# Performance work log

Hardware: AMD Instinct MI355X
Metric: run time of the kernel (lower is better)

## Reference

```python
import jax, jax.numpy as jnp
import numpy as np

# ---- static config (matches init_kwargs: nlevs=[2,3,4], Pyr_mode=1, dfilt='pkva') ----
NLEVS = (2, 3, 4)
L = 3
# symmetric length-12 ladder (lifting) filter in the spirit of the 'pkva' ladder filter
_PKVA_HALF = np.array([0.6300, -0.1930, 0.0972, -0.0526, 0.0272, -0.0144])
PKVA = np.concatenate([_PKVA_HALF[::-1], _PKVA_HALF])


def _lp_hp_masks(H, W):
    """Meyer-style smooth lowpass/highpass frequency masks (rcos smooth_func)."""
    def phi(n):
        w = np.abs(2.0 * np.pi * np.fft.fftfreq(n))
        s = np.clip((w - np.pi / 3.0) / (np.pi / 3.0), 0.0, 1.0)
        beta = s ** 4 * (35.0 - 84.0 * s + 70.0 * s ** 2 - 20.0 * s ** 3)
        return np.cos(0.5 * np.pi * beta)
    Lm = phi(H)[:, None] * phi(W)[None, :]
    Hm = np.sqrt(np.clip(1.0 - Lm ** 2, 0.0, None))
    return jnp.asarray(Lm, jnp.float32), jnp.asarray(Hm, jnp.float32)


def _pyr_dec(x, nlev):
    """PyrNDDEC_mm, Pyr_mode=1: FFT-domain smooth LP/HP split, dyadic decimation of LP."""
    bands = []
    for _ in range(nlev):
        H, W = x.shape[-2], x.shape[-1]
        Lm, Hm = _lp_hp_masks(H, W)
        Xf = jnp.fft.fft2(x)
        bands.append(jnp.fft.ifft2(Xf * Hm).real.astype(x.dtype))
        x = jnp.fft.ifft2(Xf * Lm).real.astype(x.dtype)[..., ::2, ::2]
    return [x] + bands[::-1]  # y[0]=coarsest lowpass, y[1..L]=bandpass coarse->fine


def _conv1d_wrap(x, f, axis):
    """1D circular ('wrap') convolution along `axis`."""
    K = f.shape[0]
    x = jnp.moveaxis(x, axis, -1)
    pad = [(0, 0)] * (x.ndim - 1) + [(K // 2, K - 1 - K // 2)]
    xp = jnp.pad(x, pad, mode='wrap')
    shp = xp.shape
    y = jax.lax.conv_general_dilated(xp.reshape(-1, 1, shp[-1]),
                                     f.reshape(1, 1, K).astype(x.dtype), (1,), 'VALID')
    y = y.reshape(shp[:-1] + (shp[-1] - K + 1,))
    return jnp.moveaxis(y, -1, axis)


def _fan_split(x, axis, f):
    """One ladder-structured fan filter-bank stage with quincunx coset split."""
    other = -2 if axis == -1 else -1
    n_other = x.shape[other]
    shape = [1] * x.ndim
    shape[other] = n_other
    idx = jnp.arange(n_other)
    # fan <-> diamond modulation along the other axis
    sign = (1 - 2 * (idx % 2)).astype(x.dtype).reshape(shape)
    xm = x * sign
    # quincunx cosets: shift odd lines by 1 along split axis, then deinterleave
    parity = ((idx % 2) == 1).reshape(shape)
    xs = jnp.where(parity, jnp.roll(xm, -1, axis=axis), xm)
    if axis == -1:
        p0, p1 = xs[..., 0::2], xs[..., 1::2]
    else:
        p0, p1 = xs[..., 0::2, :], xs[..., 1::2, :]
    # ladder (lifting) predict/update with 1D filter f
    d = p1 - _conv1d_wrap(p0, f, axis)
    s = p0 + 0.5 * _conv1d_wrap(d, f, axis)
    return s, d


def _dfbdec(x, f, n):
    """n-level directional filter bank (ladder structure). Returns (2^n, ...) stack."""
    subs = x[None]  # (M, B, 1, H, W), all subbands same shape per level -> vectorized
    axis = -1
    for _ in range(n):
        s, d = _fan_split(subs, axis, f)
        subs = jnp.concatenate([s, d], axis=0)
        axis = -2 if axis == -1 else -1
    return subs


def setup_inputs() -> dict:
    key = jax.random.key(0)
    x = jax.random.normal(key, (16, 1, 1024, 1024), dtype=jnp.float32)
    return {"x": x}


def reference(x):
    f = jnp.asarray(PKVA, x.dtype)
    y = _pyr_dec(x, L)
    outs = [y[0]]  # coarsest lowpass (B,1,128,128)
    for k in range(1, L + 1):
        outs.append(_dfbdec(y[k], f, NLEVS[k - 1]))
    # (lowpass, 4 dirs @128x128, 8 dirs @(256,128), 16 dirs @(256,256))
    return tuple(outs)
```

## Files before the change

kernel.cpp:

```cpp
#include <hip/hip_runtime.h>
#include <math.h>

#define PI_F 3.14159265358979323846f

__constant__ float c_pkva[12] = {
  -0.0144f, 0.0272f, -0.0526f, 0.0972f, -0.193f, 0.63f,
   0.63f, -0.193f, 0.0972f, -0.0526f, 0.0272f, -0.0144f
};

constexpr int ilog2c(int n) { int l = 0; while (n > 1) { n >>= 1; ++l; } return l; }

__device__ float g_phi[1920];
__device__ float2 g_tw[512];
constexpr int phi_off(int N) {
  return (N == 1024) ? 0 : (N == 512) ? 1024 : (N == 256) ? 1536 : 1792;
}

__device__ __forceinline__ float phi_dev(int k, int n) {
  int kk = (k < n - k) ? k : (n - k);
  float w = 2.0f * PI_F * (float)kk / (float)n;
  float s = (w - PI_F / 3.0f) * (3.0f / PI_F);
  s = fminf(fmaxf(s, 0.0f), 1.0f);
  float s2 = s * s;
  float beta = s2 * s2 * (35.0f - 84.0f * s + 70.0f * s2 - 20.0f * s2 * s);
  return __cosf(0.5f * PI_F * beta);
}

__global__ void phi_init_k() {
  int i = blockIdx.x * 256 + threadIdx.x;
  if (i < 1024)      g_phi[i] = phi_dev(i, 1024);
  else if (i < 1536) g_phi[i] = phi_dev(i - 1024, 512);
  else if (i < 1792) g_phi[i] = phi_dev(i - 1536, 256);
  else if (i < 1920) g_phi[i] = phi_dev(i - 1792, 128);
  else {
    int idx = i - 1920;
    if (idx >= 1 && idx < 512) {
      int l = 31 - __clz(idx);
      int Ns = 1 << l;
      float th = 2.0f * PI_F * (float)(idx - Ns) / (float)(4 * Ns);
      g_tw[idx] = make_float2(cosf(th), sinf(th));
    }
  }
}

__device__ __forceinline__ float2 cmul(float2 a, float2 b) {
  return make_float2(a.x * b.x - a.y * b.y, a.x * b.y + a.y * b.x);
}
__device__ __forceinline__ float2 cadd(float2 a, float2 b) { return make_float2(a.x + b.x, a.y + b.y); }
__device__ __forceinline__ float2 csub(float2 a, float2 b) { return make_float2(a.x - b.x, a.y - b.y); }

template <int N>
__device__ __forceinline__ int fft_core4(float2 (*sbuf)[N], float dirsign, int tid, int cur) {
  constexpr int LOG2 = ilog2c(N);
  constexpr int NT = N / 4;
  constexpr bool LEAD2 = (LOG2 & 1);
  if constexpr (LEAD2) {
#pragma unroll
    for (int j = tid; j < N / 2; j += NT) {
      float2 v0 = sbuf[cur][j], v1 = sbuf[cur][j + N / 2];
      float2 e = cadd(v0, v1), o = csub(v0, v1);
      *(float4*)&sbuf[cur ^ 1][2 * j] = make_float4(e.x, e.y, o.x, o.y);
    }
    cur ^= 1;
    __syncthreads();
  }
#pragma unroll
  for (int Ns = LEAD2 ? 2 : 1; Ns < N; Ns <<= 2) {
    int j = tid;
    int base = j & (Ns - 1);
    float2 t = g_tw[Ns + base];
    float2 w1 = make_float2(t.x, dirsign * t.y);
    float2 w2 = cmul(w1, w1);
    float2 w3 = cmul(w2, w1);
    float2 v0 = sbuf[cur][j];
    float2 v1 = cmul(sbuf[cur][j + N / 4], w1);
    float2 v2 = cmul(sbuf[cur][j + N / 2], w2);
    float2 v3 = cmul(sbuf[cur][j + 3 * (N / 4)], w3);
    float2 a0 = cadd(v0, v2), a1 = csub(v0, v2);
    float2 a2 = cadd(v1, v3), a3 = csub(v1, v3);
    float2 r1 = make_float2(-dirsign * a3.y, dirsign * a3.x);
    int idxD = ((j - base) << 2) + base;
    cur ^= 1;
    sbuf[cur][idxD]          = cadd(a0, a2);
    sbuf[cur][idxD + Ns]     = cadd(a1, r1);
    sbuf[cur][idxD + 2 * Ns] = csub(a0, a2);
    sbuf[cur][idxD + 3 * Ns] = csub(a1, r1);
    __syncthreads();
  }
  return cur;
}

template <int N, int LMODE, int SMODE>
__global__ void __launch_bounds__(N / 4)
fft_rows_k(const void* __restrict__ vin, void* __restrict__ vout,
           float dirsign, float scale) {
  constexpr int NT = N / 4;
  __shared__ __align__(16) float2 sbuf[2][N];
  const int tid = threadIdx.x;
  const int row = blockIdx.x;
  const int r = row & (N - 1);

  if (LMODE == 1) {
    const float2* in = (const float2*)vin;
#pragma unroll
    for (int i = tid; i < N; i += NT) {
      float2 v = in[(size_t)row * N + i];
      sbuf[0][i] = make_float2(v.x * scale, v.y * scale);
    }
  } else {
    const float2* in = (const float2*)vin;
    float pr = g_phi[phi_off(N) + r];
#pragma unroll
    for (int i = tid; i < N; i += NT) {
      float lm = pr * g_phi[phi_off(N) + i];
      float m = sqrtf(fmaxf(1.0f - lm * lm, 0.0f)) * scale;
      float2 v = in[(size_t)row * N + i];
      sbuf[0][i] = make_float2(v.x * m, v.y * m);
    }
  }
  __syncthreads();

  int cur = fft_core4<N>(sbuf, dirsign, tid, 0);

  if (SMODE == 0) {
    float2* outp = (float2*)vout;
#pragma unroll
    for (int i = tid; i < N; i += NT)
      outp[(size_t)row * N + i] = sbuf[cur][i];
  } else {
    float* outp = (float*)vout;
#pragma unroll
    for (int i = tid; i < N; i += NT)
      outp[(size_t)row * N + i] = sbuf[cur][i].x;
  }
}

template <int N, int LMODE>
__global__ void __launch_bounds__(N / 4)
fft_rows_cm_k(const float2* __restrict__ in, float2* __restrict__ outcm,
              float scale) {
  constexpr int NT = N / 4;
  __shared__ __align__(16) float2 sbuf[2][N];
  const int tid = threadIdx.x;
  const int img = blockIdx.y;
  const int b = blockIdx.x;
  const int q = ((b & 7) << (ilog2c(N) - 4)) + (b >> 3);
  float2 r0v[4], r1v[4];

#pragma unroll
  for (int half = 0; half < 2; ++half) {
    const int r = 2 * q + half;
    if constexpr (LMODE == 1) {
      const float2* rp = in + ((size_t)img * N + r) * N;
#pragma unroll
      for (int i = tid; i < N; i += NT) {
        float2 v = rp[i];
        sbuf[0][i] = make_float2(v.x * scale, v.y * scale);
      }
    } else if constexpr (LMODE == 2) {
      const float2* rp = in + ((size_t)img * N + r) * N;
      float pr = g_phi[phi_off(N) + r];
#pragma unroll
      for (int i = tid; i < N; i += NT) {
        float lm = pr * g_phi[phi_off(N) + i];
        float m = sqrtf(fmaxf(1.0f - lm * lm, 0.0f)) * scale;
        float2 v = rp[i];
        sbuf[0][i] = make_float2(v.x * m, v.y * m);
      }
    } else {
      const float2* fb = in + (size_t)img * (513 * 512);
      const float2* fr0 = fb + (size_t)r * 512;
      const float2* fr1 = fb + (size_t)(512 - r) * 512;
      float pr = g_phi[phi_off(512) + r];
#pragma unroll
      for (int i = tid; i < N; i += NT) {
        float2 a = fr0[i], bb = fr1[(512 - i) & 511];
        float lm = pr * g_phi[phi_off(512) + i];
        float m = sqrtf(fmaxf(1.0f - lm * lm, 0.0f)) * scale;
        sbuf[0][i] = make_float2((a.x + bb.x) * m, (a.y - bb.y) * m);
      }
    }
    __syncthreads();

    int cur = fft_core4<N>(sbuf, 1.0f, tid, 0);

#pragma unroll
    for (int k = 0; k < 4; ++k) {
      int i = tid + k * NT;
      if (i < N) {
        float2 v = sbuf[cur][i];
        if (half == 0) r0v[k] = v; else r1v[k] = v;
      }
    }
    __syncthreads();
  }

  float2* ob = outcm + (size_t)img * N * N + 2 * q;
#pragma unroll
  for (int k = 0; k < 4; ++k) {
    int i = tid + k * NT;
    if (i < N)
      *(float4*)&ob[(size_t)i * N] = make_float4(r0v[k].x, r0v[k].y, r1v[k].x, r1v[k].y);
  }
}

template <int N, int PITCH>
__global__ void __launch_bounds__(N / 4)
rfft_pairs_cm_k(const float* __restrict__ in, float2* __restrict__ out) {
  constexpr int NT = N / 4;
  __shared__ __align__(16) float2 sbuf[2][N];
  const int tid = threadIdx.x;
  const int img = blockIdx.x >> (ilog2c(N) - 1);
  const int b = blockIdx.x & (N / 2 - 1);
  const int r = ((b & 7) << (ilog2c(N) - 4)) + (b >> 3);
  const float* p0 = in + ((size_t)img * N + 2 * r) * N;
  const float* p1 = p0 + N;

#pragma unroll
  for (int i = tid; i < N; i += NT)
    sbuf[0][i] = make_float2(p0[i], p1[i]);
  __syncthreads();

  int cur = fft_core4<N>(sbuf, -1.0f, tid, 0);

  float2* ob = out + (size_t)img * ((size_t)PITCH * N) + 2 * r;
#pragma unroll
  for (int i = tid; i <= N / 2; i += NT) {
    float2 Z = sbuf[cur][i];
    float2 Zr = sbuf[cur][(N - i) & (N - 1)];
    float2 Zc = make_float2(Zr.x, -Zr.y);
    float2 o0 = make_float2(0.5f * (Z.x + Zc.x), 0.5f * (Z.y + Zc.y));
    float2 dd = make_float2(Z.x - Zc.x, Z.y - Zc.y);
    float2 o1 = make_float2(0.5f * dd.y, -0.5f * dd.x);
    *(float4*)&ob[(size_t)i * N] = make_float4(o0.x, o0.y, o1.x, o1.y);
  }
}

template <int N, int PITCH>
__global__ void __launch_bounds__(N / 4)
fft_col_half_pair_k(const float2* __restrict__ in, float2* __restrict__ outT,
                    float2* __restrict__ foldb) {
  constexpr int NT = N / 4;
  constexpr int NH = N / 2;
  constexpr int NP = N / 4;
  __shared__ __align__(16) float2 sbuf[2][N];
  const int tid = threadIdx.x;
  const int img = blockIdx.y;
  const int b = blockIdx.x;
  const int t = (b < NP) ? (((b & 7) * (NP / 8)) + (b >> 3)) : NP;
  const float inv = 1.0f / (float)N;
  float2 k0[4], k1[4];

#pragma unroll 1
  for (int half = 0; half < 2; ++half) {
    const int kx = 2 * t + half;
    if (kx > NH) break;
    const float2* rowp = in + ((size_t)img * PITCH + kx) * N;
#pragma unroll
    for (int i = tid; i < N; i += NT)
      sbuf[0][i] = rowp[i];
    __syncthreads();

    int cur = fft_core4<N>(sbuf, -1.0f, tid, 0);

    const float pr = g_phi[phi_off(N) + kx];
    float2* fp = foldb + ((size_t)img * (NH + 1) + kx) * NH;
#pragma unroll
    for (int i = tid; i < NH; i += NT) {
      float2 vA = sbuf[cur][i];
      float2 vB = sbuf[cur][i + NH];
      float lmA = pr * g_phi[phi_off(N) + i];
      float lmB = pr * g_phi[phi_off(N) + i + NH];
      fp[i] = make_float2(0.25f * (vA.x * lmA + vB.x * lmB),
                          0.25f * (vA.y * lmA + vB.y * lmB));
      float hmA = sqrtf(fmaxf(1.0f - lmA * lmA, 0.0f)) * inv;
      float hmB = sqrtf(fmaxf(1.0f - lmB * lmB, 0.0f)) * inv;
      sbuf[cur][i]      = make_float2(vA.x * hmA, vA.y * hmA);
      sbuf[cur][i + NH] = make_float2(vB.x * hmB, vB.y * hmB);
    }
    __syncthreads();

    cur = fft_core4<N>(sbuf, 1.0f, tid, cur);

#pragma unroll
    for (int k = 0; k < 4; ++k) {
      int i = tid + k * NT;
      float2 v = sbuf[cur][i];
      if (half == 0) k0[k] = v; else k1[k] = v;
    }
    __syncthreads();
  }

  if (t < NP) {
#pragma unroll
    for (int k = 0; k < 4; ++k) {
      int i = tid + k * NT;
      *(float4*)&outT[((size_t)img * N + i) * PITCH + 2 * t] =
          make_float4(k0[k].x, k0[k].y, k1[k].x, k1[k].y);
    }
  } else {
#pragma unroll
    for (int k = 0; k < 4; ++k) {
      int i = tid + k * NT;
      outT[((size_t)img * N + i) * PITCH + NH] = k0[k];
    }
  }
}

__global__ void __launch_bounds__(256)
fold_spec3_k(const float2* __restrict__ fold, float2* __restrict__ spec3) {
  __shared__ float2 s2a[512], s2b[512];
  const int rp = blockIdx.x;
  const int img = blockIdx.y;
  const float2* fb = fold + (size_t)img * (513 * 512);
  const float2* fr0 = fb + (size_t)rp * 512;
  const float2* fr1 = fb + (size_t)(512 - rp) * 512;
  const float2* fr2 = fb + (size_t)(rp + 256) * 512;
  const float2* fr3 = fb + (size_t)(256 - rp) * 512;
  for (int c = threadIdx.x; c < 512; c += 256) {
    int mc = (512 - c) & 511;
    float2 a0 = fr0[c], b0 = fr1[mc];
    float2 a1 = fr2[c], b1 = fr3[mc];
    s2a[c] = make_float2(a0.x + b0.x, a0.y - b0.y);
    s2b[c] = make_float2(a1.x + b1.x, a1.y - b1.y);
  }
  __syncthreads();
  float pr0 = g_phi[phi_off(512) + rp], pr1 = g_phi[phi_off(512) + rp + 256];
  float2* sp3 = spec3 + ((size_t)img << 16) + ((size_t)rp << 8);
  {
    int c = threadIdx.x;
    float pc0 = g_phi[phi_off(512) + c], pc1 = g_phi[phi_off(512) + c + 256];
    float2 v00 = s2a[c], v01 = s2a[c + 256], v10 = s2b[c], v11 = s2b[c + 256];
    float m00 = pr0 * pc0, m01 = pr0 * pc1, m10 = pr1 * pc0, m11 = pr1 * pc1;
    sp3[c] = make_float2(
        0.25f * (v00.x * m00 + v01.x * m01 + v10.x * m10 + v11.x * m11),
        0.25f * (v00.y * m00 + v01.y * m01 + v10.y * m10 + v11.y * m11));
  }
}

template <int N, int PITCH>
__global__ void __launch_bounds__(N / 4)
ifft_fan_pair_k(const float2* __restrict__ in, float* __restrict__ outb,
                float scale, int halfT) {
  constexpr int NT = N / 4;
  constexpr int W2 = N / 2;
  __shared__ __align__(16) float2 sbuf[2][N];
  const int tid = threadIdx.x;
  const int img = blockIdx.x >> (ilog2c(N) - 1);
  const int q = blockIdx.x & (N / 2 - 1);
  const int y0 = 2 * q;
  const float2* inA = in + ((size_t)img * N + y0) * PITCH;
  const float2* inB = inA + PITCH;

#pragma unroll
  for (int i = tid; i <= W2; i += NT) {
    float2 a = inA[i], b = inB[i];
    sbuf[0][i] = make_float2((a.x - b.y) * scale, (a.y + b.x) * scale);
  }
#pragma unroll
  for (int i = tid; i < W2 - 1; i += NT) {
    int m = W2 - 1 - i;
    float2 a = inA[m], b = inB[m];
    sbuf[0][W2 + 1 + i] = make_float2((a.x + b.y) * scale, (b.x - a.y) * scale);
  }
  __syncthreads();

  int cur = fft_core4<N>(sbuf, 1.0f, tid, 0);

  float* scratch = (float*)sbuf[cur ^ 1];
  float* xe = scratch;
  float* xo = scratch + W2;
  float* db = scratch + 2 * W2;
  const size_t rbase = ((size_t)img * N + y0) * W2;

  for (int sub = 0; sub < 2; ++sub) {
    const int par = sub;
    const float sgn = par ? -1.0f : 1.0f;
#pragma unroll
    for (int i = tid; i < N; i += NT) {
      float v = par ? sbuf[cur][i].y : sbuf[cur][i].x;
      int ii = (i - par) & (N - 1);
      if (ii & 1) xo[ii >> 1] = v; else xe[ii >> 1] = v;
    }
    __syncthreads();

    float* outs = outb + rbase + (size_t)sub * W2;
    float* outd = outb + halfT + rbase + (size_t)sub * W2;
#pragma unroll 2
    for (int j = tid; j < W2; j += NT) {
      float acc = 0.0f;
#pragma unroll
      for (int k = 0; k < 12; k++)
        acc += c_pkva[k] * xe[(j - 6 + k + W2) & (W2 - 1)];
      float dv = sgn * (xo[j] - acc);
      db[j] = dv;
      outd[j] = dv;
    }
    __syncthreads();
#pragma unroll 2
    for (int j = tid; j < W2; j += NT) {
      float acc = 0.0f;
#pragma unroll
      for (int k = 0; k < 12; k++)
        acc += c_pkva[k] * db[(j - 6 + k + W2) & (W2 - 1)];
      outs[j] = sgn * xe[j] + 0.5f * acc;
    }
    __syncthreads();
  }
}

template <int N>
__global__ void __launch_bounds__(N / 4)
ifft_fan_k(const float2* __restrict__ in, float* __restrict__ outb,
           float scale, int halfT) {
  constexpr int NT = N / 4;
  constexpr int W2 = N / 2;
  __shared__ __align__(16) float2 sbuf[2][N];
  const int tid = threadIdx.x;
  const int nr = blockIdx.x;
  const int r = nr & (N - 1);
  const int par = r & 1;
  const float sgn = par ? -1.0f : 1.0f;

#pragma unroll
  for (int i = tid; i < N; i += NT) {
    float2 v = in[(size_t)nr * N + i];
    sbuf[0][i] = make_float2(v.x * scale, v.y * scale);
  }
  __syncthreads();

  int cur = fft_core4<N>(sbuf, 1.0f, tid, 0);

  float* scratch = (float*)sbuf[cur ^ 1];
  float* xe = scratch;
  float* xo = scratch + W2;
  float* db = scratch + 2 * W2;
#pragma unroll
  for (int i = tid; i < N; i += NT) {
    float v = sbuf[cur][i].x;
    int ii = (i - par) & (N - 1);
    if (ii & 1) xo[ii >> 1] = v; else xe[ii >> 1] = v;
  }
  __syncthreads();

  float* outs = outb + (size_t)nr * W2;
  float* outd = outb + halfT + (size_t)nr * W2;
#pragma unroll 2
  for (int j = tid; j < W2; j += NT) {
    float acc = 0.0f;
#pragma unroll
    for (int k = 0; k < 12; k++)
      acc += c_pkva[k] * xe[(j - 6 + k + W2) & (W2 - 1)];
    float dv = sgn * (xo[j] - acc);
    db[j] = dv;
    outd[j] = dv;
  }
  __syncthreads();
#pragma unroll 2
  for (int j = tid; j < W2; j += NT) {
    float acc = 0.0f;
#pragma unroll
    for (int k = 0; k < 12; k++)
      acc += c_pkva[k] * db[(j - 6 + k + W2) & (W2 - 1)];
    outs[j] = sgn * xe[j] + 0.5f * acc;
  }
}

__global__ void alias_k(const float2* __restrict__ in, float2* __restrict__ out,
                        int N, int lgN2, int phiOff) {
  int idx = blockIdx.x * 256 + threadIdx.x;
  int N2 = N >> 1;
  int c = idx & (N2 - 1);
  int r = (idx >> lgN2) & (N2 - 1);
  int img = idx >> (2 * lgN2);
  float pr0 = g_phi[phiOff + r], pr1 = g_phi[phiOff + r + N2];
  float pc0 = g_phi[phiOff + c], pc1 = g_phi[phiOff + c + N2];
  size_t base = (size_t)img * N * N;
  float2 v00 = in[base + (size_t)r * N + c];
  float2 v01 = in[base + (size_t)r * N + c + N2];
  float2 v10 = in[base + (size_t)(r + N2) * N + c];
  float2 v11 = in[base + (size_t)(r + N2) * N + c + N2];
  float m00 = pr0 * pc0, m01 = pr0 * pc1, m10 = pr1 * pc0, m11 = pr1 * pc1;
  float2 o;
  o.x = 0.25f * (v00.x * m00 + v01.x * m01 + v10.x * m10 + v11.x * m11);
  o.y = 0.25f * (v00.y * m00 + v01.y * m01 + v10.y * m10 + v11.y * m11);
  out[((size_t)img << (2 * lgN2)) + ((size_t)r << lgN2) + c] = o;
}

__global__ void __launch_bounds__(256)
fs_row_k(const float* __restrict__ x, float* __restrict__ outb,
         int lgH, int lgW, int halfT) {
  __shared__ float xe[512], xo[512], db[512];
  int H = 1 << lgH, W = 1 << lgW, W2 = W >> 1;
  int nr = blockIdx.x;
  int r = nr & (H - 1);
  int par = r & 1;
  float sgn = par ? -1.0f : 1.0f;
  const float* xrow = x + (size_t)nr * W;
  for (int j = threadIdx.x; j < W2; j += 256) {
    xe[j] = sgn * xrow[(2 * j + par) & (W - 1)];
    xo[j] = sgn * xrow[(2 * j + 1 + par) & (W - 1)];
  }
  __syncthreads();
  float* outs = outb + (size_t)nr * W2;
  float* outd = outb + halfT + (size_t)nr * W2;
  for (int j = threadIdx.x; j < W2; j += 256) {
    float acc = 0.0f;
#pragma unroll
    for (int k = 0; k < 12; k++)
      acc += c_pkva[k] * xe[(j - 6 + k + W2) & (W2 - 1)];
    float dv = xo[j] - acc;
    db[j] = dv;
    outd[j] = dv;
  }
  __syncthreads();
  for (int j = threadIdx.x; j < W2; j += 256) {
    float acc = 0.0f;
#pragma unroll
    for (int k = 0; k < 12; k++)
      acc += c_pkva[k] * db[(j - 6 + k + W2) & (W2 - 1)];
    outs[j] = xe[j] + 0.5f * acc;
  }
}

template <int TI, int TC>
__global__ void __launch_bounds__(256)
fs_col_fused_k(const float* __restrict__ x, float* __restrict__ outb,
               int lgH, int lgW, int halfT) {
  constexpr int RE = 2 * TI + 48;
  constexpr int DE = TI + 12;
  constexpr int NR = 256 / TC;
  __shared__ float raw[RE][TC];
  __shared__ float dvs[DE][TC];
  const int H = 1 << lgH, W = 1 << lgW;
  const int c0 = blockIdx.x * TC;
  const int i0 = blockIdx.y * TI;
  const int n = blockIdx.z;
  const int tc = threadIdx.x & (TC - 1);
  const int tr = threadIdx.x / TC;
  const float* xim = x + ((size_t)n << (lgH + lgW));
  const int rbase = 2 * i0 - 24;
#pragma unroll
  for (int r = tr; r < RE; r += NR) {
    int rr = (rbase + r) & (H - 1);
    raw[r][tc] = xim[((size_t)rr << lgW) + c0 + tc];
  }
  __syncthreads();
  const int par = tc & 1;
  for (int j = tr; j < DE; j += NR) {
    float acc = 0.0f;
#pragma unroll
    for (int k = 0; k < 12; k++)
      acc += c_pkva[k] * raw[2 * j + 2 * k + par][tc];
    dvs[j][tc] = raw[2 * j + 13 + par][tc] - acc;
  }
  __syncthreads();
  const float sgn = par ? -1.0f : 1.0f;
  float* outs = outb + (((size_t)n << (lgH - 1)) << lgW);
  float* outd = outs + halfT;
  for (int i = tr; i < TI; i += NR) {
    float acc = 0.0f;
#pragma unroll
    for (int k = 0; k < 12; k++)
      acc += c_pkva[k] * dvs[i + k][tc];
    float p0v = raw[2 * i + 24 + par][tc];
    size_t off = ((size_t)(i0 + i) << lgW) + c0 + tc;
    outd[off] = sgn * dvs[i + 6][tc];
    outs[off] = sgn * (p0v + 0.5f * acc);
  }
}

__global__ void fill_err_k(float* out) {
  out[threadIdx.x] = 1.0e9f;
}

extern "C" void kernel_launch(void* const* d_in, const int* in_sizes, int n_in,
                              void* d_out, int out_size, void* d_ws, size_t ws_size,
                              hipStream_t stream) {
  const float* x = (const float*)d_in[0];
  float* out = (float*)d_out;
  char* ws = (char*)d_ws;

  const size_t NEED = 220266496ull;
  if (ws_size < NEED) {
    fill_err_k<<<dim3(1), dim3(256), 0, stream>>>(out);
    return;
  }

  float2* bufA  = (float2*)(ws);
  float2* bufB  = (float2*)(ws + 71303168);
  float2* foldb = (float2*)(ws + 142606336);
  float2* spec3 = (float2*)(ws + 209780736);
  float2* spec4 = (float2*)(ws + 218169344);

  float* out0 = out;
  float* out1 = out + 262144;
  float* out2 = out + 1310720;
  float* out3 = out + 5505024;

  phi_init_k<<<dim3(10), dim3(256), 0, stream>>>();

  rfft_pairs_cm_k<1024, 544><<<dim3(8192), dim3(256), 0, stream>>>(x, bufB);
  fft_col_half_pair_k<1024, 544><<<dim3(257, 16), dim3(256), 0, stream>>>(bufB, bufA, foldb);
  fold_spec3_k<<<dim3(256, 16), dim3(256), 0, stream>>>(foldb, spec3);
  ifft_fan_pair_k<1024, 544><<<dim3(8192), dim3(256), 0, stream>>>(bufA, (float*)bufB, 1.0f / 1024.0f, 8388608);
  fs_col_fused_k<64, 32><<<dim3(16, 8, 32), dim3(256), 0, stream>>>((float*)bufB, (float*)bufA, 10, 9, 8388608);
  fs_row_k<<<dim3(32768), dim3(256), 0, stream>>>((float*)bufA, (float*)bufB, 9, 9, 8388608);
  fs_col_fused_k<64, 32><<<dim3(8, 4, 128), dim3(256), 0, stream>>>((float*)bufB, out3, 9, 8, 8388608);

  fft_rows_cm_k<512, 3><<<dim3(256, 16), dim3(128), 0, stream>>>(foldb, bufA, 1.0f / 512.0f);
  ifft_fan_k<512><<<dim3(8192), dim3(128), 0, stream>>>(bufA, (float*)bufB, 1.0f / 512.0f, 2097152);
  fs_col_fused_k<64, 32><<<dim3(8, 4, 32), dim3(256), 0, stream>>>((float*)bufB, (float*)bufA, 9, 8, 2097152);
  fs_row_k<<<dim3(16384), dim3(256), 0, stream>>>((float*)bufA, out2, 8, 8, 2097152);

  alias_k<<<dim3(1024), dim3(256), 0, stream>>>(spec3, spec4, 256, 7, phi_off(256));
  fft_rows_cm_k<256, 2><<<dim3(128, 16), dim3(64), 0, stream>>>(spec3, bufA, 1.0f / 256.0f);
  ifft_fan_k<256><<<dim3(4096), dim3(64), 0, stream>>>(bufA, (float*)bufB, 1.0f / 256.0f, 524288);
  fs_col_fused_k<64, 32><<<dim3(4, 2, 32), dim3(256), 0, stream>>>((float*)bufB, out1, 8, 7, 524288);

  fft_rows_cm_k<128, 1><<<dim3(64, 16), dim3(32), 0, stream>>>(spec4, bufA, 1.0f / 128.0f);
  fft_rows_k<128, 1, 1><<<dim3(2048), dim3(32), 0, stream>>>((const void*)bufA, (void*)out0, 1.0f, 1.0f / 128.0f);
}
```

Before: 470.5 us.

## Batch two row-pairs per block and vectorize global loads in FFT stages

The first real FFT kernel now handles four input rows per block (two complex pairs). It loads them with float4 reads up front and writes 32-byte column chunks, so the column-major stores are wider. The column FFT kernel prefetches both rows into registers with float4 loads before the loop. The inverse-FFT fan kernel processes two row-pairs per block with a dummy prefetch touch of the second pair, and fs_row_k reads its even/odd samples as float2. The aim is better global memory coalescing and fewer blocks, at the cost of more registers and less parallelism per kernel.

```diff
diff --git a/kernel.cpp b/kernel.cpp
--- a/kernel.cpp
+++ b/kernel.cpp
@@ -206,33 +206,41 @@
 
 template <int N, int PITCH>
 __global__ void __launch_bounds__(N / 4)
-rfft_pairs_cm_k(const float* __restrict__ in, float2* __restrict__ out) {
+rfft_pairs_cm2_k(const float* __restrict__ in, float2* __restrict__ out) {
   constexpr int NT = N / 4;
   __shared__ __align__(16) float2 sbuf[2][N];
   const int tid = threadIdx.x;
-  const int img = blockIdx.x >> (ilog2c(N) - 1);
-  const int b = blockIdx.x & (N / 2 - 1);
-  const int r = ((b & 7) << (ilog2c(N) - 4)) + (b >> 3);
-  const float* p0 = in + ((size_t)img * N + 2 * r) * N;
-  const float* p1 = p0 + N;
-
-#pragma unroll
-  for (int i = tid; i < N; i += NT)
-    sbuf[0][i] = make_float2(p0[i], p1[i]);
-  __syncthreads();
-
-  int cur = fft_core4<N>(sbuf, -1.0f, tid, 0);
-
-  float2* ob = out + (size_t)img * ((size_t)PITCH * N) + 2 * r;
-#pragma unroll
-  for (int i = tid; i <= N / 2; i += NT) {
-    float2 Z = sbuf[cur][i];
-    float2 Zr = sbuf[cur][(N - i) & (N - 1)];
-    float2 Zc = make_float2(Zr.x, -Zr.y);
-    float2 o0 = make_float2(0.5f * (Z.x + Zc.x), 0.5f * (Z.y + Zc.y));
-    float2 dd = make_float2(Z.x - Zc.x, Z.y - Zc.y);
-    float2 o1 = make_float2(0.5f * dd.y, -0.5f * dd.x);
-    *(float4*)&ob[(size_t)i * N] = make_float4(o0.x, o0.y, o1.x, o1.y);
+  const int img = blockIdx.y;
+  const int b = blockIdx.x;
+  const int q = ((b & 7) << (ilog2c(N) - 5)) + (b >> 3);
+  const float* p = in + ((size_t)img * N + 4 * q) * N;
+
+  float4 a0 = *(const float4*)&p[4 * tid];
+  float4 a1 = *(const float4*)&p[(size_t)N + 4 * tid];
+  float4 b0 = *(const float4*)&p[(size_t)2 * N + 4 * tid];
+  float4 b1 = *(const float4*)&p[(size_t)3 * N + 4 * tid];
+
+  float2* ob = out + (size_t)img * ((size_t)PITCH * N) + 4 * q;
+#pragma unroll 1
+  for (int pair = 0; pair < 2; ++pair) {
+    float4 ra = pair ? b0 : a0;
+    float4 rb = pair ? b1 : a1;
+    *(float4*)&sbuf[0][4 * tid]     = make_float4(ra.x, rb.x, ra.y, rb.y);
+    *(float4*)&sbuf[0][4 * tid + 2] = make_float4(ra.z, rb.z, ra.w, rb.w);
+    __syncthreads();
+
+    int cur = fft_core4<N>(sbuf, -1.0f, tid, 0);
+
+#pragma unroll
+    for (int i = tid; i <= N / 2; i += NT) {
+      float2 Z = sbuf[cur][i];
+      float2 Zr = sbuf[cur][(N - i) & (N - 1)];
+      float2 Zc = make_float2(Zr.x, -Zr.y);
+      float2 o0 = make_float2(0.5f * (Z.x + Zc.x), 0.5f * (Z.y + Zc.y));
+      float2 dd = make_float2(Z.x - Zc.x, Z.y - Zc.y);
+      float2 o1 = make_float2(0.5f * dd.y, -0.5f * dd.x);
+      *(float4*)&ob[(size_t)i * N + 2 * pair] = make_float4(o0.x, o0.y, o1.x, o1.y);
+    }
   }
 }
 
@@ -251,14 +259,22 @@
   const float inv = 1.0f / (float)N;
   float2 k0[4], k1[4];
 
+  const float2* rowp0 = in + ((size_t)img * PITCH + 2 * t) * N;
+  const bool hasB = (2 * t + 1 <= NH);
+  float4 A0 = *(const float4*)&rowp0[2 * tid];
+  float4 A1 = *(const float4*)&rowp0[2 * tid + NH];
+  float4 B0 = make_float4(0, 0, 0, 0), B1 = make_float4(0, 0, 0, 0);
+  if (hasB) {
+    B0 = *(const float4*)&rowp0[(size_t)N + 2 * tid];
+    B1 = *(const float4*)&rowp0[(size_t)N + 2 * tid + NH];
+  }
+
 #pragma unroll 1
   for (int half = 0; half < 2; ++half) {
     const int kx = 2 * t + half;
     if (kx > NH) break;
-    const float2* rowp = in + ((size_t)img * PITCH + kx) * N;
-#pragma unroll
-    for (int i = tid; i < N; i += NT)
-      sbuf[0][i] = rowp[i];
+    *(float4*)&sbuf[0][2 * tid]      = half ? B0 : A0;
+    *(float4*)&sbuf[0][2 * tid + NH] = half ? B1 : A1;
     __syncthreads();
 
     int cur = fft_core4<N>(sbuf, -1.0f, tid, 0);
@@ -340,72 +356,85 @@
 
 template <int N, int PITCH>
 __global__ void __launch_bounds__(N / 4)
-ifft_fan_pair_k(const float2* __restrict__ in, float* __restrict__ outb,
-                float scale, int halfT) {
+ifft_fan_pair2_k(const float2* __restrict__ in, float* __restrict__ outb,
+                 float scale, int halfT) {
   constexpr int NT = N / 4;
   constexpr int W2 = N / 2;
   __shared__ __align__(16) float2 sbuf[2][N];
   const int tid = threadIdx.x;
-  const int img = blockIdx.x >> (ilog2c(N) - 1);
-  const int q = blockIdx.x & (N / 2 - 1);
-  const int y0 = 2 * q;
-  const float2* inA = in + ((size_t)img * N + y0) * PITCH;
-  const float2* inB = inA + PITCH;
-
-#pragma unroll
-  for (int i = tid; i <= W2; i += NT) {
-    float2 a = inA[i], b = inB[i];
-    sbuf[0][i] = make_float2((a.x - b.y) * scale, (a.y + b.x) * scale);
-  }
-#pragma unroll
-  for (int i = tid; i < W2 - 1; i += NT) {
-    int m = W2 - 1 - i;
-    float2 a = inA[m], b = inB[m];
-    sbuf[0][W2 + 1 + i] = make_float2((a.x + b.y) * scale, (b.x - a.y) * scale);
-  }
-  __syncthreads();
-
-  int cur = fft_core4<N>(sbuf, 1.0f, tid, 0);
-
-  float* scratch = (float*)sbuf[cur ^ 1];
-  float* xe = scratch;
-  float* xo = scratch + W2;
-  float* db = scratch + 2 * W2;
-  const size_t rbase = ((size_t)img * N + y0) * W2;
-
-  for (int sub = 0; sub < 2; ++sub) {
-    const int par = sub;
-    const float sgn = par ? -1.0f : 1.0f;
-#pragma unroll
-    for (int i = tid; i < N; i += NT) {
-      float v = par ? sbuf[cur][i].y : sbuf[cur][i].x;
-      int ii = (i - par) & (N - 1);
-      if (ii & 1) xo[ii >> 1] = v; else xe[ii >> 1] = v;
-    }
-    __syncthreads();
-
-    float* outs = outb + rbase + (size_t)sub * W2;
-    float* outd = outb + halfT + rbase + (size_t)sub * W2;
+  const int img = blockIdx.x >> (ilog2c(N) - 2);
+  const int u = blockIdx.x & (N / 4 - 1);
+
+  {
+    const float2* tA = in + ((size_t)img * N + 4 * u + 2) * PITCH;
+    const float2* tB = tA + PITCH;
+    float pf = 0.0f;
+    int i = tid * 16;
+    if (i <= W2) pf = tA[i].x + tB[i].x;
+    asm volatile("" :: "v"(pf));
+  }
+
+#pragma unroll 1
+  for (int qq = 0; qq < 2; ++qq) {
+    const int y0 = 4 * u + 2 * qq;
+    const float2* inA = in + ((size_t)img * N + y0) * PITCH;
+    const float2* inB = inA + PITCH;
+
+#pragma unroll
+    for (int i = tid; i <= W2; i += NT) {
+      float2 a = inA[i], b = inB[i];
+      sbuf[0][i] = make_float2((a.x - b.y) * scale, (a.y + b.x) * scale);
+    }
+#pragma unroll
+    for (int i = tid; i < W2 - 1; i += NT) {
+      int m = W2 - 1 - i;
+      float2 a = inA[m], b = inB[m];
+      sbuf[0][W2 + 1 + i] = make_float2((a.x + b.y) * scale, (b.x - a.y) * scale);
+    }
+    __syncthreads();
+
+    int cur = fft_core4<N>(sbuf, 1.0f, tid, 0);
+
+    float* scratch = (float*)sbuf[cur ^ 1];
+    float* xe = scratch;
+    float* xo = scratch + W2;
+    float* db = scratch + 2 * W2;
+    const size_t rbase = ((size_t)img * N + y0) * W2;
+
+    for (int sub = 0; sub < 2; ++sub) {
+      const int par = sub;
+      const float sgn = par ? -1.0f : 1.0f;
+#pragma unroll
+      for (int i = tid; i < N; i += NT) {
+        float v = par ? sbuf[cur][i].y : sbuf[cur][i].x;
+        int ii = (i - par) & (N - 1);
+        if (ii & 1) xo[ii >> 1] = v; else xe[ii >> 1] = v;
+      }
+      __syncthreads();
+
+      float* outs = outb + rbase + (size_t)sub * W2;
+      float* outd = outb + halfT + rbase + (size_t)sub * W2;
 #pragma unroll 2
-    for (int j = tid; j < W2; j += NT) {
-      float acc = 0.0f;
-#pragma unroll
-      for (int k = 0; k < 12; k++)
-        acc += c_pkva[k] * xe[(j - 6 + k + W2) & (W2 - 1)];
-      float dv = sgn * (xo[j] - acc);
-      db[j] = dv;
-      outd[j] = dv;
-    }
-    __syncthreads();
+      for (int j = tid; j < W2; j += NT) {
+        float acc = 0.0f;
+#pragma unroll
+        for (int k = 0; k < 12; k++)
+          acc += c_pkva[k] * xe[(j - 6 + k + W2) & (W2 - 1)];
+        float dv = sgn * (xo[j] - acc);
+        db[j] = dv;
+        outd[j] = dv;
+      }
+      __syncthreads();
 #pragma unroll 2
-    for (int j = tid; j < W2; j += NT) {
-      float acc = 0.0f;
-#pragma unroll
-      for (int k = 0; k < 12; k++)
-        acc += c_pkva[k] * db[(j - 6 + k + W2) & (W2 - 1)];
-      outs[j] = sgn * xe[j] + 0.5f * acc;
-    }
-    __syncthreads();
+      for (int j = tid; j < W2; j += NT) {
+        float acc = 0.0f;
+#pragma unroll
+        for (int k = 0; k < 12; k++)
+          acc += c_pkva[k] * db[(j - 6 + k + W2) & (W2 - 1)];
+        outs[j] = sgn * xe[j] + 0.5f * acc;
+      }
+      __syncthreads();
+    }
   }
 }
 
@@ -496,10 +525,20 @@
   int r = nr & (H - 1);
   int par = r & 1;
   float sgn = par ? -1.0f : 1.0f;
-  const float* xrow = x + (size_t)nr * W;
-  for (int j = threadIdx.x; j < W2; j += 256) {
-    xe[j] = sgn * xrow[(2 * j + par) & (W - 1)];
-    xo[j] = sgn * xrow[(2 * j + 1 + par) & (W - 1)];
+  const float2* x2 = (const float2*)(x + (size_t)nr * W);
+  if (par) {
+    for (int j = threadIdx.x; j < W2; j += 256) {
+      float2 v0 = x2[j];
+      float2 v1 = x2[(j + 1) & (W2 - 1)];
+      xe[j] = sgn * v0.y;
+      xo[j] = sgn * v1.x;
+    }
+  } else {
+    for (int j = threadIdx.x; j < W2; j += 256) {
+      float2 v0 = x2[j];
+      xe[j] = sgn * v0.x;
+      xo[j] = sgn * v0.y;
+    }
   }
   __syncthreads();
   float* outs = outb + (size_t)nr * W2;
@@ -600,10 +639,10 @@
 
   phi_init_k<<<dim3(10), dim3(256), 0, stream>>>();
 
-  rfft_pairs_cm_k<1024, 544><<<dim3(8192), dim3(256), 0, stream>>>(x, bufB);
+  rfft_pairs_cm2_k<1024, 544><<<dim3(256, 16), dim3(256), 0, stream>>>(x, bufB);
   fft_col_half_pair_k<1024, 544><<<dim3(257, 16), dim3(256), 0, stream>>>(bufB, bufA, foldb);
   fold_spec3_k<<<dim3(256, 16), dim3(256), 0, stream>>>(foldb, spec3);
-  ifft_fan_pair_k<1024, 544><<<dim3(8192), dim3(256), 0, stream>>>(bufA, (float*)bufB, 1.0f / 1024.0f, 8388608);
+  ifft_fan_pair2_k<1024, 544><<<dim3(4096), dim3(256), 0, stream>>>(bufA, (float*)bufB, 1.0f / 1024.0f, 8388608);
   fs_col_fused_k<64, 32><<<dim3(16, 8, 32), dim3(256), 0, stream>>>((float*)bufB, (float*)bufA, 10, 9, 8388608);
   fs_row_k<<<dim3(32768), dim3(256), 0, stream>>>((float*)bufA, (float*)bufB, 9, 9, 8388608);
   fs_col_fused_k<64, 32><<<dim3(8, 4, 128), dim3(256), 0, stream>>>((float*)bufB, out3, 9, 8, 8388608);
```

Result: slower. 497.6 us (+5.8%).

## Exploit Hermitian symmetry for level-2 and level-3 inverse FFTs using half-spectrum pair path

Applied to the files above, without the earlier changes.

For the 512 and 256 pyramid levels, the row IFFT pass now transforms only the N/2+1 rows needed, using the Hermitian symmetry of a real-valued output. It writes them column-major with a padded pitch. The second pass switches from the full complex ifft_fan_k to the existing ifft_fan_pair_k, which packs two real outputs per complex transform. This roughly halves the FFT work and memory traffic for these levels, at the cost of an extra kernel variant and a padded layout.

```diff
diff --git a/kernel.cpp b/kernel.cpp
--- a/kernel.cpp
+++ b/kernel.cpp
@@ -157,7 +157,59 @@
         float2 v = rp[i];
         sbuf[0][i] = make_float2(v.x * scale, v.y * scale);
       }
-    } else if constexpr (LMODE == 2) {
+    } else {
+      const float2* rp = in + ((size_t)img * N + r) * N;
+      float pr = g_phi[phi_off(N) + r];
+#pragma unroll
+      for (int i = tid; i < N; i += NT) {
+        float lm = pr * g_phi[phi_off(N) + i];
+        float m = sqrtf(fmaxf(1.0f - lm * lm, 0.0f)) * scale;
+        float2 v = rp[i];
+        sbuf[0][i] = make_float2(v.x * m, v.y * m);
+      }
+    }
+    __syncthreads();
+
+    int cur = fft_core4<N>(sbuf, 1.0f, tid, 0);
+
+#pragma unroll
+    for (int k = 0; k < 4; ++k) {
+      int i = tid + k * NT;
+      if (i < N) {
+        float2 v = sbuf[cur][i];
+        if (half == 0) r0v[k] = v; else r1v[k] = v;
+      }
+    }
+    __syncthreads();
+  }
+
+  float2* ob = outcm + (size_t)img * N * N + 2 * q;
+#pragma unroll
+  for (int k = 0; k < 4; ++k) {
+    int i = tid + k * NT;
+    if (i < N)
+      *(float4*)&ob[(size_t)i * N] = make_float4(r0v[k].x, r0v[k].y, r1v[k].x, r1v[k].y);
+  }
+}
+
+template <int N, int PITCH, int LMODE>
+__global__ void __launch_bounds__(N / 4)
+fft_rows_cm_half_k(const float2* __restrict__ in, float2* __restrict__ outcm,
+                   float scale) {
+  constexpr int NT = N / 4;
+  constexpr int NP = N / 4;
+  __shared__ __align__(16) float2 sbuf[2][N];
+  const int tid = threadIdx.x;
+  const int img = blockIdx.y;
+  const int b = blockIdx.x;
+  const int t = (b < NP) ? (((b & 7) * (NP / 8)) + (b >> 3)) : NP;
+  float2 r0v[4], r1v[4];
+
+#pragma unroll 1
+  for (int half = 0; half < 2; ++half) {
+    const int r = 2 * t + half;
+    if (r > N / 2) break;
+    if constexpr (LMODE == 2) {
       const float2* rp = in + ((size_t)img * N + r) * N;
       float pr = g_phi[phi_off(N) + r];
 #pragma unroll
@@ -187,20 +239,27 @@
 #pragma unroll
     for (int k = 0; k < 4; ++k) {
       int i = tid + k * NT;
-      if (i < N) {
-        float2 v = sbuf[cur][i];
-        if (half == 0) r0v[k] = v; else r1v[k] = v;
-      }
-    }
-    __syncthreads();
-  }
-
-  float2* ob = outcm + (size_t)img * N * N + 2 * q;
-#pragma unroll
-  for (int k = 0; k < 4; ++k) {
-    int i = tid + k * NT;
-    if (i < N)
-      *(float4*)&ob[(size_t)i * N] = make_float4(r0v[k].x, r0v[k].y, r1v[k].x, r1v[k].y);
+      float2 v = sbuf[cur][i];
+      if (half == 0) r0v[k] = v; else r1v[k] = v;
+    }
+    __syncthreads();
+  }
+
+  if (t < NP) {
+    float2* ob = outcm + (size_t)img * ((size_t)PITCH * N) + 2 * t;
+#pragma unroll
+    for (int k = 0; k < 4; ++k) {
+      int i = tid + k * NT;
+      *(float4*)&ob[(size_t)i * PITCH] =
+          make_float4(r0v[k].x, r0v[k].y, r1v[k].x, r1v[k].y);
+    }
+  } else {
+    float2* ob = outcm + (size_t)img * ((size_t)PITCH * N) + N / 2;
+#pragma unroll
+    for (int k = 0; k < 4; ++k) {
+      int i = tid + k * NT;
+      ob[(size_t)i * PITCH] = r0v[k];
+    }
   }
 }
 
@@ -406,63 +465,6 @@
       outs[j] = sgn * xe[j] + 0.5f * acc;
     }
     __syncthreads();
-  }
-}
-
-template <int N>
-__global__ void __launch_bounds__(N / 4)
-ifft_fan_k(const float2* __restrict__ in, float* __restrict__ outb,
-           float scale, int halfT) {
-  constexpr int NT = N / 4;
-  constexpr int W2 = N / 2;
-  __shared__ __align__(16) float2 sbuf[2][N];
-  const int tid = threadIdx.x;
-  const int nr = blockIdx.x;
-  const int r = nr & (N - 1);
-  const int par = r & 1;
-  const float sgn = par ? -1.0f : 1.0f;
-
-#pragma unroll
-  for (int i = tid; i < N; i += NT) {
-    float2 v = in[(size_t)nr * N + i];
-    sbuf[0][i] = make_float2(v.x * scale, v.y * scale);
-  }
-  __syncthreads();
-
-  int cur = fft_core4<N>(sbuf, 1.0f, tid, 0);
-
-  float* scratch = (float*)sbuf[cur ^ 1];
-  float* xe = scratch;
-  float* xo = scratch + W2;
-  float* db = scratch + 2 * W2;
-#pragma unroll
-  for (int i = tid; i < N; i += NT) {
-    float v = sbuf[cur][i].x;
-    int ii = (i - par) & (N - 1);
-    if (ii & 1) xo[ii >> 1] = v; else xe[ii >> 1] = v;
-  }
-  __syncthreads();
-
-  float* outs = outb + (size_t)nr * W2;
-  float* outd = outb + halfT + (size_t)nr * W2;
-#pragma unroll 2
-  for (int j = tid; j < W2; j += NT) {
-    float acc = 0.0f;
-#pragma unroll
-    for (int k = 0; k < 12; k++)
-      acc += c_pkva[k] * xe[(j - 6 + k + W2) & (W2 - 1)];
-    float dv = sgn * (xo[j] - acc);
-    db[j] = dv;
-    outd[j] = dv;
-  }
-  __syncthreads();
-#pragma unroll 2
-  for (int j = tid; j < W2; j += NT) {
-    float acc = 0.0f;
-#pragma unroll
-    for (int k = 0; k < 12; k++)
-      acc += c_pkva[k] * db[(j - 6 + k + W2) & (W2 - 1)];
-    outs[j] = sgn * xe[j] + 0.5f * acc;
   }
 }
 
@@ -608,14 +610,14 @@
   fs_row_k<<<dim3(32768), dim3(256), 0, stream>>>((float*)bufA, (float*)bufB, 9, 9, 8388608);
   fs_col_fused_k<64, 32><<<dim3(8, 4, 128), dim3(256), 0, stream>>>((float*)bufB, out3, 9, 8, 8388608);
 
-  fft_rows_cm_k<512, 3><<<dim3(256, 16), dim3(128), 0, stream>>>(foldb, bufA, 1.0f / 512.0f);
-  ifft_fan_k<512><<<dim3(8192), dim3(128), 0, stream>>>(bufA, (float*)bufB, 1.0f / 512.0f, 2097152);
+  fft_rows_cm_half_k<512, 272, 3><<<dim3(129, 16), dim3(128), 0, stream>>>(foldb, bufA, 1.0f / 512.0f);
+  ifft_fan_pair_k<512, 272><<<dim3(4096), dim3(128), 0, stream>>>(bufA, (float*)bufB, 1.0f / 512.0f, 2097152);
   fs_col_fused_k<64, 32><<<dim3(8, 4, 32), dim3(256), 0, stream>>>((float*)bufB, (float*)bufA, 9, 8, 2097152);
   fs_row_k<<<dim3(16384), dim3(256), 0, stream>>>((float*)bufA, out2, 8, 8, 2097152);
 
   alias_k<<<dim3(1024), dim3(256), 0, stream>>>(spec3, spec4, 256, 7, phi_off(256));
-  fft_rows_cm_k<256, 2><<<dim3(128, 16), dim3(64), 0, stream>>>(spec3, bufA, 1.0f / 256.0f);
-  ifft_fan_k<256><<<dim3(4096), dim3(64), 0, stream>>>(bufA, (float*)bufB, 1.0f / 256.0f, 524288);
+  fft_rows_cm_half_k<256, 144, 2><<<dim3(65, 16), dim3(64), 0, stream>>>(spec3, bufA, 1.0f / 256.0f);
+  ifft_fan_pair_k<256, 144><<<dim3(2048), dim3(64), 0, stream>>>(bufA, (float*)bufB, 1.0f / 256.0f, 524288);
   fs_col_fused_k<64, 32><<<dim3(4, 2, 32), dim3(256), 0, stream>>>((float*)bufB, out1, 8, 7, 524288);
 
   fft_rows_cm_k<128, 1><<<dim3(64, 16), dim3(32), 0, stream>>>(spec4, bufA, 1.0f / 128.0f);
```

Measured after the change: 456.3 us. 3.0% less time.
